# Kernel tuning notes

Hardware: AMD Instinct MI355X
Metric: run time of the kernel (lower is better)

The kernel has to match this reference:

```python
import jax, jax.numpy as jnp
import numpy as np

POOL_H, POOL_W = 7, 7


def setup_inputs() -> dict:
    key = jax.random.key(0)
    k1, k2 = jax.random.split(key)
    B, C, H, W, N, BOX_DIM = 4, 64, 128, 128, 64, 7
    feat = jax.random.normal(k1, (B, C, H, W), dtype=jnp.float32)
    # box coords in feature-map pixel units; cols 0:4 = x1,y1,x2,y2, rest extras
    boxes = jax.random.uniform(k2, (B, N, BOX_DIM), dtype=jnp.float32) * (W - 1)
    # make the first box of each batch all-zero -> exercises the invalid-box zero-fill path
    boxes = boxes.at[:, 0, :].set(0.0)
    return {"spatial_features": feat, "boxes": boxes}


def _roi_pool(feat, boxes):
    # feat: [B, C, H, W]; boxes: [B, N, >=4]
    B, C, H, W = feat.shape
    b = jax.lax.stop_gradient(boxes)
    # clamp to feature bounds (same as torch.clamp in the original)
    x1 = jnp.clip(b[..., 0], 0, W - 1)
    y1 = jnp.clip(b[..., 1], 0, H - 1)
    x2 = jnp.clip(b[..., 2], 0, W - 1)
    y2 = jnp.clip(b[..., 3], 0, H - 1)
    # replicate original (buggy-but-faithful) ordering: x1 updated first, then x2 uses new x1
    x1 = jnp.minimum(x1, x2)
    x2 = jnp.maximum(x1, x2)
    y1 = jnp.minimum(y1, y2)
    y2 = jnp.maximum(y1, y2)
    # .int() truncation (coords are non-negative after clamp -> floor)
    x1i = x1.astype(jnp.int32)
    x2i = x2.astype(jnp.int32)
    y1i = y1.astype(jnp.int32)
    y2i = y2.astype(jnp.int32)
    x2i = jnp.where(x2i == x1i, x1i + 1, x2i)
    y2i = jnp.where(y2i == y1i, y1i + 1, y2i)
    Lh = y2i - y1i  # [B, N] roi heights (>=1)
    Lw = x2i - x1i  # [B, N] roi widths  (>=1)

    hs = jnp.arange(H)
    ws = jnp.arange(W)
    ninf = -jnp.inf

    # adaptive_max_pool2d bin boundaries: start = floor(p*L/P), end = ceil((p+1)*L/P)
    # stage 1: pool over rows (y) -> [B, N, POOL_H, C, W]
    rows = []
    for p in range(POOL_H):
        s = y1i + (p * Lh) // POOL_H
        e = y1i + ((p + 1) * Lh + POOL_H - 1) // POOL_H
        m = (hs[None, None, :] >= s[..., None]) & (hs[None, None, :] < e[..., None])  # [B,N,H]
        v = jnp.where(m[:, :, None, :, None], feat[:, None], ninf)  # [B,N,C,H,W] (fused under jit)
        rows.append(v.max(axis=3))  # [B,N,C,W]
    py = jnp.stack(rows, axis=2)  # [B, N, POOL_H, C, W]

    # stage 2: pool over cols (x) -> [B, N, POOL_H, C] per bin
    cols = []
    for q in range(POOL_W):
        s = x1i + (q * Lw) // POOL_W
        e = x1i + ((q + 1) * Lw + POOL_W - 1) // POOL_W
        m = (ws[None, None, :] >= s[..., None]) & (ws[None, None, :] < e[..., None])  # [B,N,W]
        v = jnp.where(m[:, :, None, None, :], py, ninf)  # [B,N,POOL_H,C,W]
        cols.append(v.max(axis=-1))  # [B,N,POOL_H,C]
    out = jnp.stack(cols, axis=-1)  # [B, N, POOL_H, C, POOL_W]
    out = jnp.transpose(out, (0, 1, 3, 2, 4))  # [B, N, C, POOL_H, POOL_W]

    # invalid (all-zero) boxes produce zeros, like the original's zero fill
    valid = jnp.any(boxes != 0, axis=-1)  # [B, N]
    return jnp.where(valid[:, :, None, None, None], out, 0.0)


def reference(spatial_features, boxes):
    return _roi_pool(spatial_features, boxes)
```

## Files before the change

kernel.cpp:

```cpp
#include <hip/hip_runtime.h>


constexpr int Bb = 4, Cc = 64, Hh = 128, Ww = 128, Nn = 64, BOX_DIM = 7;
constexpr int POOL = 7;
constexpr int WAVES = 8;
constexpr int PITCH = Ww + 1;

__global__ __launch_bounds__(512) void roi_pool_kernel(
    const float* __restrict__ feat,
    const float* __restrict__ boxes,
    float* __restrict__ out)
{
    __shared__ float colmax[WAVES][POOL][PITCH];

    const int bn   = blockIdx.y;
    const int b    = bn >> 6;
    const int wave = threadIdx.x >> 6;
    const int lane = threadIdx.x & 63;
    const int c    = blockIdx.x * WAVES + wave;

    const float* bx = boxes + (size_t)bn * BOX_DIM;
    bool valid = false;
#pragma unroll
    for (int i = 0; i < BOX_DIM; ++i) valid = valid || (bx[i] != 0.0f);

    float x1 = fminf(fmaxf(bx[0], 0.0f), (float)(Ww - 1));
    float y1 = fminf(fmaxf(bx[1], 0.0f), (float)(Hh - 1));
    float x2 = fminf(fmaxf(bx[2], 0.0f), (float)(Ww - 1));
    float y2 = fminf(fmaxf(bx[3], 0.0f), (float)(Hh - 1));
    x1 = fminf(x1, x2);
    x2 = fmaxf(x1, x2);
    y1 = fminf(y1, y2);
    y2 = fmaxf(y1, y2);

    int x1i = __builtin_amdgcn_readfirstlane((int)x1);
    int x2i = __builtin_amdgcn_readfirstlane((int)x2);
    int y1i = __builtin_amdgcn_readfirstlane((int)y1);
    int y2i = __builtin_amdgcn_readfirstlane((int)y2);
    if (x2i == x1i) x2i = x1i + 1;
    if (y2i == y1i) y2i = y1i + 1;
    const int Lh = y2i - y1i;
    const int Lw = x2i - x1i;
    const int ylast = y2i - 1;

    const float* fp = feat + ((size_t)(b * Cc + c) * Hh) * Ww;

    for (int x0 = 0; x0 < Lw; x0 += 64) {
        const int xoff = x0 + lane;
        const int xcol = x1i + min(xoff, Lw - 1);

        float buf[8];
#pragma unroll
        for (int j = 0; j < 8; ++j)
            buf[j] = fp[(size_t)(min(y1i + j, ylast) * Ww) + xcol];

        int   p_cur = 0;
        int   e_cur = y1i + (Lh + POOL - 1) / POOL;
        float cur   = -INFINITY;
        float prev  = -INFINITY;
        int   y     = y1i;

        const int ngroups = (Lh + 7) >> 3;
        for (int g = 0; g < ngroups; ++g) {
#pragma unroll
            for (int j = 0; j < 8; ++j) {
                const float v = buf[j];
                buf[j] = fp[(size_t)(min(y + 8, ylast) * Ww) + xcol];
                while (y >= e_cur) {
                    colmax[wave][p_cur][xoff] = cur;
                    ++p_cur;
                    const int s_new = y1i + (p_cur * Lh) / POOL;
                    cur = (s_new == y - 1) ? prev : -INFINITY;
                    e_cur = (p_cur == POOL - 1)
                                ? 0x7fffffff
                                : (y1i + ((p_cur + 1) * Lh + POOL - 1) / POOL);
                }
                cur  = fmaxf(cur, v);
                prev = v;
                ++y;
            }
        }
        colmax[wave][p_cur][xoff] = cur;
        for (int p = p_cur + 1; p < POOL; ++p)
            colmax[wave][p][xoff] = prev;
    }

    __syncthreads();

    if (lane < POOL * POOL) {
        const int p = lane / POOL;
        const int q = lane % POOL;
        const int xs = (q * Lw) / POOL;
        const int xe = ((q + 1) * Lw + POOL - 1) / POOL;
        float m = -INFINITY;
        for (int xo = xs; xo < xe; ++xo)
            m = fmaxf(m, colmax[wave][p][xo]);
        if (!valid) m = 0.0f;
        out[((size_t)bn * Cc + c) * (POOL * POOL) + lane] = m;
    }
}

extern "C" void kernel_launch(void* const* d_in, const int* in_sizes, int n_in,
                              void* d_out, int out_size, void* d_ws, size_t ws_size,
                              hipStream_t stream) {
    const float* feat  = (const float*)d_in[0];
    const float* boxes = (const float*)d_in[1];
    float* out = (float*)d_out;

    dim3 grid(Cc / WAVES, Bb * Nn);
    roi_pool_kernel<<<grid, 512, 0, stream>>>(feat, boxes, out);
}
```

Measured before the change: 25.28 us.

## Split ROI row scan across four waves per channel to shorten serial chains

Each block now handles 2 channels instead of 8, and the ROI's rows are split into 4 segments, each scanned by its own wave. Per-segment partial column maxima go to shared memory and are combined in the final column-pooling step. Bin boundaries are precomputed into small arrays, and the prefetch depth drops from 8 to 4. The goal is more parallelism and a shorter per-wave serial load chain. The cost is 4x more blocks, redundant box parsing per block, and extra shared-memory initialization and reduction work.

Result: slower. 37.39 us (+47.9%).

```diff
diff --git a/kernel.cpp b/kernel.cpp
--- a/kernel.cpp
+++ b/kernel.cpp
@@ -3,7 +3,8 @@
 
 constexpr int Bb = 4, Cc = 64, Hh = 128, Ww = 128, Nn = 64, BOX_DIM = 7;
 constexpr int POOL = 7;
-constexpr int WAVES = 8;
+constexpr int CH_PER = 2;
+constexpr int YS = 4;
 constexpr int PITCH = Ww + 1;
 
 __global__ __launch_bounds__(512) void roi_pool_kernel(
@@ -11,13 +12,15 @@
     const float* __restrict__ boxes,
     float* __restrict__ out)
 {
-    __shared__ float colmax[WAVES][POOL][PITCH];
+    __shared__ float colmax[CH_PER][YS][POOL][PITCH];
 
     const int bn   = blockIdx.y;
     const int b    = bn >> 6;
     const int wave = threadIdx.x >> 6;
     const int lane = threadIdx.x & 63;
-    const int c    = blockIdx.x * WAVES + wave;
+    const int ch   = wave & 1;
+    const int seg  = wave >> 1;
+    const int c    = blockIdx.x * CH_PER + ch;
 
     const float* bx = boxes + (size_t)bn * BOX_DIM;
     bool valid = false;
@@ -41,7 +44,16 @@
     if (y2i == y1i) y2i = y1i + 1;
     const int Lh = y2i - y1i;
     const int Lw = x2i - x1i;
-    const int ylast = y2i - 1;
+
+    int s_[POOL], e_[POOL];
+#pragma unroll
+    for (int p = 0; p < POOL; ++p) {
+        s_[p] = y1i + (p * Lh) / POOL;
+        e_[p] = y1i + ((p + 1) * Lh + POOL - 1) / POOL;
+    }
+
+    const int ys = y1i + (seg * Lh) / YS;
+    const int ye = y1i + ((seg + 1) * Lh) / YS;
 
     const float* fp = feat + ((size_t)(b * Cc + c) * Hh) * Ww;
 
@@ -49,54 +61,82 @@
         const int xoff = x0 + lane;
         const int xcol = x1i + min(xoff, Lw - 1);
 
-        float buf[8];
 #pragma unroll
-        for (int j = 0; j < 8; ++j)
-            buf[j] = fp[(size_t)(min(y1i + j, ylast) * Ww) + xcol];
+        for (int p = 0; p < POOL; ++p)
+            colmax[ch][seg][p][xoff] = -INFINITY;
 
-        int   p_cur = 0;
-        int   e_cur = y1i + (Lh + POOL - 1) / POOL;
-        float cur   = -INFINITY;
-        float prev  = -INFINITY;
-        int   y     = y1i;
+        if (ys < ye) {
+            int p_cur = 0;
+            while (e_[p_cur] <= ys) ++p_cur;
+            int   e_cur = e_[p_cur];
+            float cur   = -INFINITY;
+            float prev  = -INFINITY;
 
-        const int ngroups = (Lh + 7) >> 3;
-        for (int g = 0; g < ngroups; ++g) {
+            const int yl = ye - 1;
+            float buf[4];
 #pragma unroll
-            for (int j = 0; j < 8; ++j) {
-                const float v = buf[j];
-                buf[j] = fp[(size_t)(min(y + 8, ylast) * Ww) + xcol];
+            for (int j = 0; j < 4; ++j)
+                buf[j] = fp[(size_t)(min(ys + j, yl) * Ww) + xcol];
+
+            int y = ys;
+            const int nfull = (ye - ys) >> 2;
+            for (int g = 0; g < nfull; ++g) {
+#pragma unroll
+                for (int j = 0; j < 4; ++j) {
+                    const float v = buf[j];
+                    buf[j] = fp[(size_t)(min(y + 4, yl) * Ww) + xcol];
+                    while (y >= e_cur) {
+                        colmax[ch][seg][p_cur][xoff] = cur;
+                        ++p_cur;
+                        cur   = (s_[p_cur] == y - 1) ? prev : -INFINITY;
+                        e_cur = e_[p_cur];
+                    }
+                    cur  = fmaxf(cur, v);
+                    prev = v;
+                    ++y;
+                }
+            }
+            const int rem = (ye - ys) & 3;
+            for (int k = 0; k < rem; ++k) {
+                const float v = buf[k];
                 while (y >= e_cur) {
-                    colmax[wave][p_cur][xoff] = cur;
+                    colmax[ch][seg][p_cur][xoff] = cur;
                     ++p_cur;
-                    const int s_new = y1i + (p_cur * Lh) / POOL;
-                    cur = (s_new == y - 1) ? prev : -INFINITY;
-                    e_cur = (p_cur == POOL - 1)
-                                ? 0x7fffffff
-                                : (y1i + ((p_cur + 1) * Lh + POOL - 1) / POOL);
+                    cur   = (s_[p_cur] == y - 1) ? prev : -INFINITY;
+                    e_cur = e_[p_cur];
                 }
                 cur  = fmaxf(cur, v);
                 prev = v;
                 ++y;
             }
+
+            colmax[ch][seg][p_cur][xoff] = cur;
+#pragma unroll
+            for (int p = 1; p < POOL; ++p)
+                if (p > p_cur && s_[p] == ye - 1)
+                    colmax[ch][seg][p][xoff] = prev;
         }
-        colmax[wave][p_cur][xoff] = cur;
-        for (int p = p_cur + 1; p < POOL; ++p)
-            colmax[wave][p][xoff] = prev;
     }
 
     __syncthreads();
 
-    if (lane < POOL * POOL) {
-        const int p = lane / POOL;
-        const int q = lane % POOL;
-        const int xs = (q * Lw) / POOL;
-        const int xe = ((q + 1) * Lw + POOL - 1) / POOL;
+    const int t = threadIdx.x;
+    if (t < CH_PER * POOL * POOL) {
+        const int chh = t / (POOL * POOL);
+        const int pq  = t % (POOL * POOL);
+        const int p   = pq / POOL;
+        const int q   = pq % POOL;
+        const int xs  = (q * Lw) / POOL;
+        const int xe  = ((q + 1) * Lw + POOL - 1) / POOL;
         float m = -INFINITY;
-        for (int xo = xs; xo < xe; ++xo)
-            m = fmaxf(m, colmax[wave][p][xo]);
+        for (int xo = xs; xo < xe; ++xo) {
+#pragma unroll
+            for (int sg = 0; sg < YS; ++sg)
+                m = fmaxf(m, colmax[chh][sg][p][xo]);
+        }
         if (!valid) m = 0.0f;
-        out[((size_t)bn * Cc + c) * (POOL * POOL) + lane] = m;
+        const int cc = blockIdx.x * CH_PER + chh;
+        out[((size_t)bn * Cc + cc) * (POOL * POOL) + pq] = m;
     }
 }
 
@@ -107,6 +147,6 @@
     const float* boxes = (const float*)d_in[1];
     float* out = (float*)d_out;
 
-    dim3 grid(Cc / WAVES, Bb * Nn);
+    dim3 grid(Cc / CH_PER, Bb * Nn);
     roi_pool_kernel<<<grid, 512, 0, stream>>>(feat, boxes, out);
 }
```
